# Kernel optimization log

Measured on AMD Instinct MI355X. Metric: run time of the kernel, lower is better.

The kernel has to match this reference:

```python
import jax, jax.numpy as jnp
import numpy as np

N = 100000
E = 1600000
IN_CH = 128
HID = 128
HEADS = 4
C = HID // HEADS  # 32 per-head channels
NUM_CLASSES = 40
NEG_SLOPE = 0.2


def _glorot(key, shape):
    fan_in, fan_out = shape[0], shape[-1]
    lim = jnp.sqrt(6.0 / (fan_in + fan_out))
    return jax.random.uniform(key, shape, jnp.float32, -lim, lim)


def setup_inputs() -> dict:
    key = jax.random.key(0)
    ks = jax.random.split(key, 12)
    x = jax.random.normal(ks[0], (N, IN_CH), jnp.float32)
    edge_index = jax.random.randint(ks[1], (2, E), 0, N, jnp.int64)
    edge_weight = jax.random.uniform(ks[2], (E,), jnp.float32)
    return {
        'x': x,
        'edge_index': edge_index,
        'edge_weight': edge_weight,
        'W_pre': _glorot(ks[3], (IN_CH, HID)),
        'Wl': _glorot(ks[4], (HID, HEADS * C)),
        'bl': jnp.zeros((HEADS * C,), jnp.float32),
        'Wr': _glorot(ks[5], (HID, HEADS * C)),
        'br': jnp.zeros((HEADS * C,), jnp.float32),
        'We': _glorot(ks[6], (1, HEADS * C)),
        'att': _glorot(ks[7], (HEADS, C)),
        'b_gat': jnp.zeros((HEADS * C,), jnp.float32),
        'W1': _glorot(ks[8], (HID, HID)),
        'b1': jnp.zeros((HID,), jnp.float32),
        'W2': _glorot(ks[9], (HID, NUM_CLASSES)),
        'b2': jnp.zeros((NUM_CLASSES,), jnp.float32),
    }


def reference(x, edge_index, edge_weight, W_pre, Wl, bl, Wr, br, We, att, b_gat, W1, b1, W2, b2):
    # pre projection (bias=False), norm = Identity
    h0 = x @ W_pre  # [N, HID]

    # --- GATv2Conv (PyG semantics, eval mode) ---
    # add self loops; self-loop edge_attr = mean of existing edge_attr (fill_value='mean')
    loop = jnp.arange(N, dtype=edge_index.dtype)
    src = jnp.concatenate([edge_index[0], loop])  # [E+N]
    dst = jnp.concatenate([edge_index[1], loop])
    ea = jnp.concatenate([edge_weight, jnp.full((N,), jnp.mean(edge_weight), edge_weight.dtype)])  # [E+N]

    x_l = (h0 @ Wl + bl).reshape(N, HEADS, C)  # source transform
    x_r = (h0 @ Wr + br).reshape(N, HEADS, C)  # target transform
    edge_emb = (ea[:, None] * We).reshape(-1, HEADS, C)  # lin_edge (bias=False)

    xj = x_l[src]  # [Etot, H, C] gather of source features
    e = jax.nn.leaky_relu(xj + x_r[dst] + edge_emb, NEG_SLOPE)
    alpha = jnp.einsum('ehc,hc->eh', e, att)  # [Etot, H]

    # segment softmax over destination neighborhoods
    amax = jax.ops.segment_max(alpha, dst, num_segments=N)
    amax = jnp.where(jnp.isfinite(amax), amax, 0.0)
    ex = jnp.exp(alpha - amax[dst])
    denom = jax.ops.segment_sum(ex, dst, num_segments=N)
    attn = ex / (denom[dst] + 1e-16)  # [Etot, H]

    out = jax.ops.segment_sum(attn[:, :, None] * xj, dst, num_segments=N)  # [N, H, C]
    out = out.reshape(N, HEADS * C) + b_gat

    h1 = jax.nn.elu(out)
    h = h0 + h1  # residual

    logits = jax.nn.relu(h @ W1 + b1) @ W2 + b2
    return h, logits
```

## Files before the change

### kernel.cpp

```cpp
#include <hip/hip_runtime.h>

typedef __attribute__((ext_vector_type(8))) short short8;
typedef __attribute__((ext_vector_type(16))) float f32x16;

#if __has_builtin(__builtin_amdgcn_exp2f)
#define EXP2(x) __builtin_amdgcn_exp2f(x)
#else
#define EXP2(x) exp2f(x)
#endif

static __device__ __forceinline__ unsigned short f2bf(float f){
  unsigned u = __float_as_uint(f);
  unsigned r = u + 0x7fffu + ((u >> 16) & 1u);
  return (unsigned short)(r >> 16);
}
static __device__ __forceinline__ float bf2f(unsigned short h){
  return __uint_as_float(((unsigned)h) << 16);
}

__global__ void wprep(const float* __restrict__ Wpre, const float* __restrict__ W1,
                      const float* __restrict__ W2, const float* __restrict__ bl,
                      const float* __restrict__ br,
                      unsigned short* __restrict__ PhiF, unsigned short* __restrict__ PloF,
                      unsigned short* __restrict__ W1hiF, unsigned short* __restrict__ W1loF,
                      unsigned short* __restrict__ W2hiF, unsigned short* __restrict__ W2loF,
                      float* __restrict__ bcat){
  int i = blockIdx.x*256 + threadIdx.x;
  float v; unsigned short* hp; unsigned short* lp; size_t idx;
  if (i < 16384){
    int k = i >> 7, c = i & 127;
    v = Wpre[i]; hp = PhiF; lp = PloF;
    idx = ((size_t)(k>>3)*128 + c)*8 + (k&7);
  } else if (i < 32768){
    int j = i - 16384; int k = j >> 7, c = j & 127;
    v = W1[j]; hp = W1hiF; lp = W1loF;
    idx = ((size_t)(k>>3)*128 + c)*8 + (k&7);
  } else if (i < 37888){
    int j = i - 32768; int k = j / 40, c = j % 40;
    v = W2[j]; hp = W2hiF; lp = W2loF;
    idx = ((size_t)(k>>3)*40 + c)*8 + (k&7);
  } else if (i < 38144){
    int j = i - 37888;
    bcat[j] = (j < 128) ? bl[j] : br[j-128];
    return;
  } else return;
  unsigned short h = f2bf(v);
  hp[idx] = h;
  lp[idx] = f2bf(v - bf2f(h));
}

__global__ __launch_bounds__(256) void wcomb_kernel(
    const float* __restrict__ Wpre, const float* __restrict__ Wl,
    const float* __restrict__ Wr,
    unsigned short* __restrict__ ChiF, unsigned short* __restrict__ CloF){
  int tid = blockIdx.x*256 + threadIdx.x;
  int r = tid >> 8;
  int c = tid & 255;
  const float* B = (c < 128) ? (Wl + c) : (Wr + (c - 128));
  float s = 0.f;
  for (int k = 0; k < 128; ++k)
    s = fmaf(Wpre[r*128 + k], B[(size_t)k*128], s);
  unsigned short h = f2bf(s);
  size_t idx = ((size_t)(r>>3)*256 + c)*8 + (r&7);
  ChiF[idx] = h;
  CloF[idx] = f2bf(s - bf2f(h));
}

__global__ void count_mean(const int* __restrict__ ei, const float* __restrict__ ew,
                           int* __restrict__ deg, int* __restrict__ rk,
                           float* __restrict__ msum, int E){
  float s = 0.f;
  for (int e = blockIdx.x*256 + threadIdx.x; e < E; e += gridDim.x*256){
    rk[e] = atomicAdd(&deg[ei[E + e]], 1);
    s += ew[e];
  }
  for (int d = 32; d > 0; d >>= 1) s += __shfl_down(s, d, 64);
  __shared__ float ps[4];
  int lane = threadIdx.x & 63, w = threadIdx.x >> 6;
  if (lane == 0) ps[w] = s;
  __syncthreads();
  if (threadIdx.x == 0) atomicAdd(msum, (ps[0]+ps[1]+ps[2]+ps[3]) / (float)E);
}

__global__ __launch_bounds__(256) void scan1_kernel(const int* __restrict__ deg, int* __restrict__ rowptr,
                                                    int* __restrict__ bsum, int* __restrict__ dhist, int N){
  __shared__ int s[256];
  __shared__ int lhist[256];
  int i = blockIdx.x*256 + threadIdx.x;
  lhist[threadIdx.x] = 0;
  __syncthreads();
  int v = (i < N) ? deg[i] : 0;
  if (i < N) atomicAdd(&lhist[v < 255 ? v : 255], 1);
  s[threadIdx.x] = v;
  __syncthreads();
  for (int off = 1; off < 256; off <<= 1){
    int t = (threadIdx.x >= off) ? s[threadIdx.x - off] : 0;
    __syncthreads();
    s[threadIdx.x] += t;
    __syncthreads();
  }
  if (i < N) rowptr[i + 1] = s[threadIdx.x];
  if (threadIdx.x == 255) bsum[blockIdx.x] = s[255];
  int c = lhist[threadIdx.x];
  if (c > 0) atomicAdd(&dhist[threadIdx.x], c);
}

__global__ __launch_bounds__(512) void scan2_kernel(const int* __restrict__ bsum, int* __restrict__ boff, int nb,
                                                    const int* __restrict__ dhist, int* __restrict__ dhoff){
  __shared__ int s[512];
  __shared__ int s2[256];
  int v = (threadIdx.x < nb) ? bsum[threadIdx.x] : 0;
  s[threadIdx.x] = v;
  __syncthreads();
  for (int off = 1; off < 512; off <<= 1){
    int t = (threadIdx.x >= off) ? s[threadIdx.x - off] : 0;
    __syncthreads();
    s[threadIdx.x] += t;
    __syncthreads();
  }
  if (threadIdx.x < nb) boff[threadIdx.x] = s[threadIdx.x] - v;
  int v2 = 0;
  if (threadIdx.x < 256){ v2 = dhist[threadIdx.x]; s2[threadIdx.x] = v2; }
  __syncthreads();
  for (int off = 1; off < 256; off <<= 1){
    int t = 0;
    if (threadIdx.x < 256 && threadIdx.x >= off) t = s2[threadIdx.x - off];
    __syncthreads();
    if (threadIdx.x < 256) s2[threadIdx.x] += t;
    __syncthreads();
  }
  if (threadIdx.x < 256) dhoff[threadIdx.x] = s2[threadIdx.x] - v2;
}

__global__ __launch_bounds__(256) void scan3_kernel(int* __restrict__ rowptr, const int* __restrict__ boff,
                                                    const int* __restrict__ deg, int* __restrict__ dhoff,
                                                    int* __restrict__ perm, int N){
  __shared__ int lcnt[256];
  __shared__ int lbase[256];
  int i = blockIdx.x*256 + threadIdx.x;
  lcnt[threadIdx.x] = 0;
  __syncthreads();
  if (i == 0) rowptr[0] = 0;
  int d = 0, lr = 0;
  if (i < N){
    rowptr[i + 1] += boff[i >> 8];
    d = deg[i]; d = d < 255 ? d : 255;
    lr = atomicAdd(&lcnt[d], 1);
  }
  __syncthreads();
  int c = lcnt[threadIdx.x];
  if (c > 0) lbase[threadIdx.x] = atomicAdd(&dhoff[threadIdx.x], c);
  __syncthreads();
  if (i < N) perm[lbase[d] + lr] = i;
}

__global__ void fill_kernel(const int* __restrict__ ei, const float* __restrict__ ew,
                            const int* __restrict__ rowptr, const int* __restrict__ rk,
                            int2* __restrict__ erec, int E){
  int e = blockIdx.x*256 + threadIdx.x;
  if (e >= E) return;
  int dst = ei[E + e];
  erec[rowptr[dst] + rk[e]] = make_int2(ei[e], __float_as_int(ew[e]));
}

template<int NT>
static __device__ __forceinline__ void stageA(short* alds, const float* __restrict__ A,
                                              int row0, int N, int t){
  for (int g = t; g < 1024; g += NT){
    int r = g >> 4, k8 = g & 15;
    int grow = row0 + r;
    float4 p0, p1;
    if (grow < N){
      const float* ap = A + (size_t)grow*128 + k8*8;
      p0 = *(const float4*)ap;
      p1 = *(const float4*)(ap + 4);
    } else {
      p0 = make_float4(0.f,0.f,0.f,0.f); p1 = p0;
    }
    float vv[8] = {p0.x,p0.y,p0.z,p0.w,p1.x,p1.y,p1.z,p1.w};
    short8 hv, lv;
    #pragma unroll
    for (int j = 0; j < 8; ++j){
      unsigned short h = f2bf(vv[j]);
      hv[j] = (short)h;
      lv[j] = (short)f2bf(vv[j] - bf2f(h));
    }
    int slot = k8 ^ (r & 15);
    *(short8*)&alds[r*128 + slot*8] = hv;
    *(short8*)&alds[8192 + r*128 + slot*8] = lv;
  }
}

#define MFMA_KLOOP(ACC0, ACC1) \
  _Pragma("unroll") \
  for (int ks = 0; ks < 8; ++ks){ \
    int k8 = ks*2 + kg; \
    const short* a0 = &alds[r0*128 + (k8 ^ sx)*8]; \
    const short* a1 = &alds[(r0+32)*128 + (k8 ^ sx)*8]; \
    short8 a0h = *(const short8*)a0; \
    short8 a0l = *(const short8*)(a0 + 8192); \
    short8 a1h = *(const short8*)a1; \
    short8 a1l = *(const short8*)(a1 + 8192); \
    ACC0 = __builtin_amdgcn_mfma_f32_32x32x16_bf16(a0h, bh[ks],  ACC0, 0,0,0); \
    ACC1 = __builtin_amdgcn_mfma_f32_32x32x16_bf16(a1h, bh[ks],  ACC1, 0,0,0); \
    ACC0 = __builtin_amdgcn_mfma_f32_32x32x16_bf16(a0l, bh[ks],  ACC0, 0,0,0); \
    ACC1 = __builtin_amdgcn_mfma_f32_32x32x16_bf16(a1l, bh[ks],  ACC1, 0,0,0); \
    ACC0 = __builtin_amdgcn_mfma_f32_32x32x16_bf16(a0h, bl8[ks], ACC0, 0,0,0); \
    ACC1 = __builtin_amdgcn_mfma_f32_32x32x16_bf16(a1h, bl8[ks], ACC1, 0,0,0); \
  }

__global__ __launch_bounds__(768) void pre_kernel(
    const float* __restrict__ A,
    const unsigned short* __restrict__ PhiF, const unsigned short* __restrict__ PloF,
    const unsigned short* __restrict__ ChiF, const unsigned short* __restrict__ CloF,
    const float* __restrict__ bcat,
    float* __restrict__ hout, unsigned short* __restrict__ xlr, int N)
{
  __shared__ short alds[2*64*128];
  const int t = threadIdx.x;
  const int row0 = blockIdx.x * 64;
  const int lane = t & 63, w = t >> 6;
  const int cl = lane & 31, kg = lane >> 5;
  const int sx = cl & 15;
  const int S = w * 32;
  const bool isP = S < 128;
  const int col = isP ? (S + cl) : (S - 128 + cl);
  const int NC  = isP ? 128 : 256;
  const unsigned short* Bhi = isP ? PhiF : ChiF;
  const unsigned short* Blo = isP ? PloF : CloF;

  short8 bh[8], bl8[8];
  #pragma unroll
  for (int ks = 0; ks < 8; ++ks){
    size_t off = ((size_t)(ks*2 + kg)*NC + col)*8;
    bh[ks]  = *(const short8*)(Bhi + off);
    bl8[ks] = *(const short8*)(Blo + off);
  }

  stageA<768>(alds, A, row0, N, t);
  __syncthreads();

  f32x16 acc0, acc1;
  #pragma unroll
  for (int i = 0; i < 16; ++i){ acc0[i] = 0.f; acc1[i] = 0.f; }
  const int r0 = cl;
  MFMA_KLOOP(acc0, acc1)

  if (isP){
    #pragma unroll
    for (int rt2 = 0; rt2 < 2; ++rt2){
      const f32x16& ac = rt2 ? acc1 : acc0;
      #pragma unroll
      for (int reg = 0; reg < 16; ++reg){
        int row = rt2*32 + (reg & 3) + 8*(reg >> 2) + 4*kg;
        int grow = row0 + row;
        if (grow < N) hout[(size_t)grow*128 + col] = ac[reg];
      }
    }
  } else {
    float bv = bcat[col];
    #pragma unroll
    for (int rt2 = 0; rt2 < 2; ++rt2){
      const f32x16& ac = rt2 ? acc1 : acc0;
      #pragma unroll
      for (int reg = 0; reg < 16; ++reg){
        int row = rt2*32 + (reg & 3) + 8*(reg >> 2) + 4*kg;
        int grow = row0 + row;
        if (grow < N) xlr[(size_t)grow*256 + col] = f2bf(ac[reg] + bv);
      }
    }
  }
}

__global__ __launch_bounds__(256) void mlp_kernel(
    const float* __restrict__ A,
    const unsigned short* __restrict__ B1hi, const unsigned short* __restrict__ B1lo,
    const float* __restrict__ b1,
    const unsigned short* __restrict__ B2hi, const unsigned short* __restrict__ B2lo,
    const float* __restrict__ b2,
    float* __restrict__ logits, int N)
{
  __shared__ short alds[2*64*128];
  const int t = threadIdx.x;
  const int row0 = blockIdx.x * 64;
  stageA<256>(alds, A, row0, N, t);
  __syncthreads();

  const int lane = t & 63, w = t >> 6;
  const int cl = lane & 31, kg = lane >> 5;
  const int r0 = cl;
  const int sx = r0 & 15;

  {
    const int col = w*32 + cl;
    short8 bh[8], bl8[8];
    #pragma unroll
    for (int ks = 0; ks < 8; ++ks){
      size_t off = ((size_t)(ks*2 + kg)*128 + col)*8;
      bh[ks]  = *(const short8*)(B1hi + off);
      bl8[ks] = *(const short8*)(B1lo + off);
    }
    f32x16 acc0, acc1;
    #pragma unroll
    for (int i = 0; i < 16; ++i){ acc0[i] = 0.f; acc1[i] = 0.f; }
    MFMA_KLOOP(acc0, acc1)

    float bv = b1[col];
    __syncthreads();
    #pragma unroll
    for (int rt = 0; rt < 2; ++rt){
      const f32x16& ac = rt ? acc1 : acc0;
      #pragma unroll
      for (int reg = 0; reg < 16; ++reg){
        int row = rt*32 + (reg & 3) + 8*(reg >> 2) + 4*kg;
        float v = fmaxf(ac[reg] + bv, 0.f);
        unsigned short h = f2bf(v);
        unsigned short l = f2bf(v - bf2f(h));
        int idx = row*128 + (((col >> 3) ^ (row & 15)) << 3) + (col & 7);
        alds[idx] = (short)h;
        alds[8192 + idx] = (short)l;
      }
    }
    __syncthreads();
  }

  if (w < 2){
    const int col = w*32 + cl;
    const bool cok = col < 40;
    short8 bh[8], bl8[8];
    #pragma unroll
    for (int ks = 0; ks < 8; ++ks){
      if (cok){
        size_t off = ((size_t)(ks*2 + kg)*40 + col)*8;
        bh[ks]  = *(const short8*)(B2hi + off);
        bl8[ks] = *(const short8*)(B2lo + off);
      } else {
        #pragma unroll
        for (int j = 0; j < 8; ++j){ bh[ks][j] = 0; bl8[ks][j] = 0; }
      }
    }
    f32x16 acc0, acc1;
    #pragma unroll
    for (int i = 0; i < 16; ++i){ acc0[i] = 0.f; acc1[i] = 0.f; }
    MFMA_KLOOP(acc0, acc1)

    if (cok){
      float bv = b2[col];
      #pragma unroll
      for (int rt = 0; rt < 2; ++rt){
        const f32x16& ac = rt ? acc1 : acc0;
        #pragma unroll
        for (int reg = 0; reg < 16; ++reg){
          int row = rt*32 + (reg & 3) + 8*(reg >> 2) + 4*kg;
          int grow = row0 + row;
          if (grow < N) logits[(size_t)grow*40 + col] = ac[reg] + bv;
        }
      }
    }
  }
}

__global__ __launch_bounds__(256) void gather_kernel(
    const int* __restrict__ rowptr, const int2* __restrict__ erec,
    const unsigned short* __restrict__ xlr,
    const int* __restrict__ perm,
    const float* __restrict__ We, const float* __restrict__ att,
    const float* __restrict__ msum, const float* __restrict__ bgat,
    float* __restrict__ hbuf, int N)
{
  const int wid  = threadIdx.x >> 6;
  const int lane = threadIdx.x & 63;
  const int g    = lane >> 4;
  const int l    = lane & 15;
  const int ch0  = l * 8;
  const int slot = (blockIdx.x*4 + wid)*4 + g;
  const bool nok = slot < N;
  const int n    = nok ? perm[slot] : 0;

  float xrv[8], wev[8], at6[8], at4[8];
  {
    short8 q = *(const short8*)&xlr[(size_t)n*256 + 128 + ch0];
    float4 w0 = *(const float4*)&We[ch0];
    float4 w1 = *(const float4*)&We[ch0+4];
    float4 a0 = *(const float4*)&att[ch0];
    float4 a1 = *(const float4*)&att[ch0+4];
    const float L2E = 1.4426950408889634f;
    float wv[8] = {w0.x,w0.y,w0.z,w0.w,w1.x,w1.y,w1.z,w1.w};
    float av[8] = {a0.x,a0.y,a0.z,a0.w,a1.x,a1.y,a1.z,a1.w};
    #pragma unroll
    for (int j = 0; j < 8; ++j){
      xrv[j] = bf2f((unsigned short)q[j]);
      wev[j] = wv[j];
      at6[j] = av[j]*0.6f*L2E;
      at4[j] = av[j]*0.4f*L2E;
    }
  }

  float num[8];
  #pragma unroll
  for (int j = 0; j < 8; ++j) num[j] = 0.f;
  float den = 0.f;

  const float wm = msum[0];
  int beg = 0, end = 0;
  if (nok){ beg = rowptr[n]; end = rowptr[n + 1]; }
  const int cnt = nok ? (end - beg + 1) : 0;

  int itMax = cnt;
  itMax = max(itMax, __shfl_xor(itMax, 16, 64));
  itMax = max(itMax, __shfl_xor(itMax, 32, 64));

  const int2 selfrec = make_int2(n, __float_as_int(wm));

  int pos = beg;
  int2 rec0 = (pos     < end) ? erec[pos]     : selfrec;
  int2 rec1 = (pos + 1 < end) ? erec[pos + 1] : selfrec;
  int2 rec2 = (pos + 2 < end) ? erec[pos + 2] : selfrec;
  short8 pv0 = *(const short8*)&xlr[(size_t)rec0.x*256 + ch0];
  short8 pv1 = *(const short8*)&xlr[(size_t)rec1.x*256 + ch0];
  short8 pv2 = *(const short8*)&xlr[(size_t)rec2.x*256 + ch0];

  for (int it = 0; it < itMax; it += 2){
    int2 rec3 = (pos + 3 < end) ? erec[pos + 3] : selfrec;
    int2 rec4 = (pos + 4 < end) ? erec[pos + 4] : selfrec;
    short8 pv3 = *(const short8*)&xlr[(size_t)rec3.x*256 + ch0];
    short8 pv4 = *(const short8*)&xlr[(size_t)rec4.x*256 + ch0];

    {
      const bool act = it < cnt;
      const float wj = __int_as_float(rec0.y);
      float xlv[8];
      #pragma unroll
      for (int q = 0; q < 8; ++q) xlv[q] = bf2f((unsigned short)pv0[q]);
      float p = 0.f;
      #pragma unroll
      for (int q = 0; q < 8; ++q){
        float z = fmaf(wj, wev[q], xlv[q] + xrv[q]);
        p = fmaf(at6[q], z, p);
        p = fmaf(at4[q], fabsf(z), p);
      }
      p += __shfl_xor(p, 1, 64);
      p += __shfl_xor(p, 2, 64);
      float ex = act ? EXP2(p) : 0.f;
      den += ex;
      #pragma unroll
      for (int q = 0; q < 8; ++q) num[q] = fmaf(ex, xlv[q], num[q]);
    }
    {
      const bool act = (it + 1) < cnt;
      const float wj = __int_as_float(rec1.y);
      float xlv[8];
      #pragma unroll
      for (int q = 0; q < 8; ++q) xlv[q] = bf2f((unsigned short)pv1[q]);
      float p = 0.f;
      #pragma unroll
      for (int q = 0; q < 8; ++q){
        float z = fmaf(wj, wev[q], xlv[q] + xrv[q]);
        p = fmaf(at6[q], z, p);
        p = fmaf(at4[q], fabsf(z), p);
      }
      p += __shfl_xor(p, 1, 64);
      p += __shfl_xor(p, 2, 64);
      float ex = act ? EXP2(p) : 0.f;
      den += ex;
      #pragma unroll
      for (int q = 0; q < 8; ++q) num[q] = fmaf(ex, xlv[q], num[q]);
    }

    rec0 = rec2; rec1 = rec3; rec2 = rec4;
    pv0 = pv2;  pv1 = pv3;  pv2 = pv4;
    pos += 2;
  }

  if (nok){
    float inv = 1.f / (den + 1e-16f);
    float o[8];
    #pragma unroll
    for (int j = 0; j < 8; ++j){
      float v = num[j]*inv + bgat[ch0+j];
      o[j] = v > 0.f ? v : expm1f(v);
    }
    float4 h0a = *(const float4*)&hbuf[(size_t)n*128 + ch0];
    float4 h0b = *(const float4*)&hbuf[(size_t)n*128 + ch0 + 4];
    h0a.x += o[0]; h0a.y += o[1]; h0a.z += o[2]; h0a.w += o[3];
    h0b.x += o[4]; h0b.y += o[5]; h0b.z += o[6]; h0b.w += o[7];
    *(float4*)&hbuf[(size_t)n*128 + ch0]     = h0a;
    *(float4*)&hbuf[(size_t)n*128 + ch0 + 4] = h0b;
  }
}

extern "C" void kernel_launch(void* const* d_in, const int* in_sizes, int n_in,
                              void* d_out, int out_size, void* d_ws, size_t ws_size,
                              hipStream_t stream)
{
  const float* x    = (const float*)d_in[0];
  const int*   ei   = (const int*)  d_in[1];
  const float* ew   = (const float*)d_in[2];
  const float* Wpre = (const float*)d_in[3];
  const float* Wl   = (const float*)d_in[4];
  const float* bl   = (const float*)d_in[5];
  const float* Wr   = (const float*)d_in[6];
  const float* br   = (const float*)d_in[7];
  const float* We   = (const float*)d_in[8];
  const float* att  = (const float*)d_in[9];
  const float* bgat = (const float*)d_in[10];
  const float* W1   = (const float*)d_in[11];
  const float* b1   = (const float*)d_in[12];
  const float* W2   = (const float*)d_in[13];
  const float* b2   = (const float*)d_in[14];

  const int N = in_sizes[0] / 128;
  const int E = in_sizes[2];
  const int nb = (N + 255) / 256;

  float* hout   = (float*)d_out;
  float* logits = hout + (size_t)N*128;

  unsigned short* xlr = (unsigned short*)d_ws;
  int2*  erec   = (int2*)(xlr + (size_t)N*256);
  int*   rk     = (int*)(erec + E);
  int*   rowptr = rk + E;
  int*   cursor = rowptr + N + 1;
  float* msum   = (float*)(cursor + N);
  int*   dhist  = (int*)(msum + 1);
  int*   bsum   = dhist + 256;
  int*   boff   = bsum + nb;
  int*   dhoff  = boff + nb;
  int*   perm   = dhoff + 256;
  float* bcat   = (float*)(perm + N);
  unsigned short* wsp = (unsigned short*)(((uintptr_t)(bcat + 256) + 15) & ~(uintptr_t)15);
  unsigned short* PhiF  = wsp;
  unsigned short* PloF  = PhiF + 16384;
  unsigned short* ChiF  = PloF + 16384;
  unsigned short* CloF  = ChiF + 32768;
  unsigned short* W1hiF = CloF + 32768;
  unsigned short* W1loF = W1hiF + 16384;
  unsigned short* W2hiF = W1loF + 16384;
  unsigned short* W2loF = W2hiF + 5120;

  hipMemsetAsync(cursor, 0, (size_t)(N + 1 + 256) * sizeof(int), stream);

  wprep<<<150, 256, 0, stream>>>(Wpre, W1, W2, bl, br,
                                 PhiF, PloF, W1hiF, W1loF, W2hiF, W2loF, bcat);
  wcomb_kernel<<<128, 256, 0, stream>>>(Wpre, Wl, Wr, ChiF, CloF);
  count_mean<<<1024, 256, 0, stream>>>(ei, ew, cursor, rk, msum, E);
  scan1_kernel<<<nb, 256, 0, stream>>>(cursor, rowptr, bsum, dhist, N);
  scan2_kernel<<<1, 512, 0, stream>>>(bsum, boff, nb, dhist, dhoff);
  scan3_kernel<<<nb, 256, 0, stream>>>(rowptr, boff, cursor, dhoff, perm, N);
  fill_kernel<<<(E + 255)/256, 256, 0, stream>>>(ei, ew, rowptr, rk, erec, E);

  const int gg = (N + 63) / 64;
  pre_kernel<<<gg, 768, 0, stream>>>(x, PhiF, PloF, ChiF, CloF, bcat, hout, xlr, N);

  gather_kernel<<<(N + 15)/16, 256, 0, stream>>>(rowptr, erec, xlr, perm, We, att, msum, bgat, hout, N);

  mlp_kernel<<<gg, 256, 0, stream>>>(hout, W1hiF, W1loF, b1, W2hiF, W2loF, b2, logits, N);
}
```

Measured before the change: 319.4 us.

## Make pre_kernel persistent with double-buffered LDS prefetch of input tiles

The pre-projection GEMM kernel now launches a fixed grid of 512 blocks that loop over 64-row tiles. Each block keeps its bf16 hi/lo weight fragments in registers across tiles, and the global loads for the next tile are issued before computing the current one, with the split written into a second LDS buffer. This targets per-block weight reload and launch overhead, and hides global load latency behind the MFMA work. In exchange it doubles LDS use to 64 KB per block and raises register pressure from the prefetch registers, which may limit occupancy.

After: 299.3 us. -6.3%, faster.

```diff
diff --git a/kernel.cpp b/kernel.cpp
--- a/kernel.cpp
+++ b/kernel.cpp
@@ -214,11 +214,10 @@
     const unsigned short* __restrict__ PhiF, const unsigned short* __restrict__ PloF,
     const unsigned short* __restrict__ ChiF, const unsigned short* __restrict__ CloF,
     const float* __restrict__ bcat,
-    float* __restrict__ hout, unsigned short* __restrict__ xlr, int N)
+    float* __restrict__ hout, unsigned short* __restrict__ xlr, int N, int ntiles)
 {
-  __shared__ short alds[2*64*128];
+  __shared__ short sh[2][16384];
   const int t = threadIdx.x;
-  const int row0 = blockIdx.x * 64;
   const int lane = t & 63, w = t >> 6;
   const int cl = lane & 31, kg = lane >> 5;
   const int sx = cl & 15;
@@ -228,6 +227,7 @@
   const int NC  = isP ? 128 : 256;
   const unsigned short* Bhi = isP ? PhiF : ChiF;
   const unsigned short* Blo = isP ? PloF : CloF;
+  const float bv = isP ? 0.f : bcat[col];
 
   short8 bh[8], bl8[8];
   #pragma unroll
@@ -237,38 +237,99 @@
     bl8[ks] = *(const short8*)(Blo + off);
   }
 
-  stageA<768>(alds, A, row0, N, t);
-  __syncthreads();
-
-  f32x16 acc0, acc1;
-  #pragma unroll
-  for (int i = 0; i < 16; ++i){ acc0[i] = 0.f; acc1[i] = 0.f; }
-  const int r0 = cl;
-  MFMA_KLOOP(acc0, acc1)
-
-  if (isP){
-    #pragma unroll
-    for (int rt2 = 0; rt2 < 2; ++rt2){
-      const f32x16& ac = rt2 ? acc1 : acc0;
-      #pragma unroll
-      for (int reg = 0; reg < 16; ++reg){
-        int row = rt2*32 + (reg & 3) + 8*(reg >> 2) + 4*kg;
-        int grow = row0 + row;
-        if (grow < N) hout[(size_t)grow*128 + col] = ac[reg];
-      }
-    }
-  } else {
-    float bv = bcat[col];
-    #pragma unroll
-    for (int rt2 = 0; rt2 < 2; ++rt2){
-      const f32x16& ac = rt2 ? acc1 : acc0;
-      #pragma unroll
-      for (int reg = 0; reg < 16; ++reg){
-        int row = rt2*32 + (reg & 3) + 8*(reg >> 2) + 4*kg;
-        int grow = row0 + row;
-        if (grow < N) xlr[(size_t)grow*256 + col] = f2bf(ac[reg] + bv);
-      }
-    }
+  const int r_0 = t >> 4,         k8_0 = t & 15;
+  const int g1  = t + 768;
+  const int r_1 = g1 >> 4,        k8_1 = g1 & 15;
+  const bool has1 = g1 < 1024;
+  float4 pa0, pa1, pb0, pb1;
+
+  auto LOAD = [&](int tl){
+    int row0 = tl*64;
+    int gr = row0 + r_0;
+    if (gr < N){ const float* ap = A + (size_t)gr*128 + k8_0*8; pa0 = *(const float4*)ap; pa1 = *(const float4*)(ap+4); }
+    else { pa0 = make_float4(0.f,0.f,0.f,0.f); pa1 = pa0; }
+    if (has1){
+      int gr1 = row0 + r_1;
+      if (gr1 < N){ const float* ap = A + (size_t)gr1*128 + k8_1*8; pb0 = *(const float4*)ap; pb1 = *(const float4*)(ap+4); }
+      else { pb0 = make_float4(0.f,0.f,0.f,0.f); pb1 = pb0; }
+    }
+  };
+  auto STORE = [&](short* buf){
+    {
+      float vv[8] = {pa0.x,pa0.y,pa0.z,pa0.w,pa1.x,pa1.y,pa1.z,pa1.w};
+      short8 hv, lv;
+      #pragma unroll
+      for (int j = 0; j < 8; ++j){
+        unsigned short h = f2bf(vv[j]);
+        hv[j] = (short)h;
+        lv[j] = (short)f2bf(vv[j] - bf2f(h));
+      }
+      int slot = k8_0 ^ (r_0 & 15);
+      *(short8*)&buf[r_0*128 + slot*8] = hv;
+      *(short8*)&buf[8192 + r_0*128 + slot*8] = lv;
+    }
+    if (has1){
+      float vv[8] = {pb0.x,pb0.y,pb0.z,pb0.w,pb1.x,pb1.y,pb1.z,pb1.w};
+      short8 hv, lv;
+      #pragma unroll
+      for (int j = 0; j < 8; ++j){
+        unsigned short h = f2bf(vv[j]);
+        hv[j] = (short)h;
+        lv[j] = (short)f2bf(vv[j] - bf2f(h));
+      }
+      int slot = k8_1 ^ (r_1 & 15);
+      *(short8*)&buf[r_1*128 + slot*8] = hv;
+      *(short8*)&buf[8192 + r_1*128 + slot*8] = lv;
+    }
+  };
+  auto COMPUTE = [&](int tl, const short* alds){
+    f32x16 acc0, acc1;
+    #pragma unroll
+    for (int i = 0; i < 16; ++i){ acc0[i] = 0.f; acc1[i] = 0.f; }
+    const int r0 = cl;
+    MFMA_KLOOP(acc0, acc1)
+    int row0 = tl*64;
+    if (isP){
+      #pragma unroll
+      for (int rt2 = 0; rt2 < 2; ++rt2){
+        const f32x16& ac = rt2 ? acc1 : acc0;
+        #pragma unroll
+        for (int reg = 0; reg < 16; ++reg){
+          int row = rt2*32 + (reg & 3) + 8*(reg >> 2) + 4*kg;
+          int grow = row0 + row;
+          if (grow < N) hout[(size_t)grow*128 + col] = ac[reg];
+        }
+      }
+    } else {
+      #pragma unroll
+      for (int rt2 = 0; rt2 < 2; ++rt2){
+        const f32x16& ac = rt2 ? acc1 : acc0;
+        #pragma unroll
+        for (int reg = 0; reg < 16; ++reg){
+          int row = rt2*32 + (reg & 3) + 8*(reg >> 2) + 4*kg;
+          int grow = row0 + row;
+          if (grow < N) xlr[(size_t)grow*256 + col] = f2bf(ac[reg] + bv);
+        }
+      }
+    }
+  };
+
+  int tile = blockIdx.x;
+  if (tile >= ntiles) return;
+  LOAD(tile);
+  STORE(sh[0]);
+  __syncthreads();
+  int cur = 0;
+  while (true){
+    int next = tile + gridDim.x;
+    bool more = next < ntiles;
+    if (more) LOAD(next);
+    COMPUTE(tile, sh[cur]);
+    if (!more) break;
+    STORE(sh[cur^1]);
+    __syncthreads();
+    cur ^= 1;
+    tile = next;
   }
 }
 
@@ -549,10 +610,10 @@
   scan3_kernel<<<nb, 256, 0, stream>>>(rowptr, boff, cursor, dhoff, perm, N);
   fill_kernel<<<(E + 255)/256, 256, 0, stream>>>(ei, ew, rowptr, rk, erec, E);
 
-  const int gg = (N + 63) / 64;
-  pre_kernel<<<gg, 768, 0, stream>>>(x, PhiF, PloF, ChiF, CloF, bcat, hout, xlr, N);
+  const int ntiles = (N + 63) / 64;
+  pre_kernel<<<512, 768, 0, stream>>>(x, PhiF, PloF, ChiF, CloF, bcat, hout, xlr, N, ntiles);
 
   gather_kernel<<<(N + 15)/16, 256, 0, stream>>>(rowptr, erec, xlr, perm, We, att, msum, bgat, hout, N);
 
-  mlp_kernel<<<gg, 256, 0, stream>>>(hout, W1hiF, W1loF, b1, W2hiF, W2loF, b2, logits, N);
-}
+  mlp_kernel<<<(N + 63)/64, 256, 0, stream>>>(hout, W1hiF, W1loF, b1, W2hiF, W2loF, b2, logits, N);
+}
```
